# Performance work log

Hardware: AMD Instinct MI355X
Metric: run time of the kernel (lower is better)

The kernel has to match this reference:

```python
import jax, jax.numpy as jnp
import numpy as np

# Mamba2 config (from AdapterMamba: d_model=1024, n_layer=4, headdim=32; mamba_ssm defaults)
D_MODEL = 1024
N_LAYER = 4
EXPAND = 2
HEADDIM = 32
D_STATE = 128
D_CONV = 4
NGROUPS = 1
D_INNER = EXPAND * D_MODEL            # 2048
NHEADS = D_INNER // HEADDIM           # 64
CONV_DIM = D_INNER + 2 * NGROUPS * D_STATE   # 2304
D_IN_PROJ = 2 * D_INNER + 2 * NGROUPS * D_STATE + NHEADS  # 4416
BATCH, SEQLEN = 4, 2048


def setup_inputs() -> dict:
    key = jax.random.key(0)
    ks = jax.random.split(key, 8)
    x = jax.random.normal(ks[0], (BATCH, SEQLEN, D_MODEL), jnp.float32)
    s_in = 1.0 / np.sqrt(D_MODEL)
    s_out = 1.0 / np.sqrt(D_INNER)
    W_in = jax.random.normal(ks[1], (N_LAYER, D_MODEL, D_IN_PROJ), jnp.float32) * s_in
    conv_w = jax.random.normal(ks[2], (N_LAYER, CONV_DIM, D_CONV), jnp.float32) * 0.5
    conv_b = jnp.zeros((N_LAYER, CONV_DIM), jnp.float32)
    # dt_bias = softplus^{-1}(dt) for dt in [1e-3, 0.1] (mamba dt_init)
    dt = jax.random.uniform(ks[3], (N_LAYER, NHEADS), jnp.float32, 0.001, 0.1)
    dt_bias = jnp.log(jnp.expm1(dt))
    # A in [1, 16] per head (A_init_range)
    A_log = jnp.log(jax.random.uniform(ks[4], (N_LAYER, NHEADS), jnp.float32, 1.0, 16.0))
    D = jnp.ones((N_LAYER, NHEADS), jnp.float32)
    gate_norm_w = jnp.ones((N_LAYER, D_INNER), jnp.float32)
    W_out = jax.random.normal(ks[5], (N_LAYER, D_INNER, D_MODEL), jnp.float32) * s_out
    block_norm_w = jnp.ones((N_LAYER, D_MODEL), jnp.float32)
    final_norm_w = jnp.ones((D_MODEL,), jnp.float32)
    return dict(x=x, W_in=W_in, conv_w=conv_w, conv_b=conv_b, dt_bias=dt_bias,
                A_log=A_log, D=D, gate_norm_w=gate_norm_w, W_out=W_out,
                block_norm_w=block_norm_w, final_norm_w=final_norm_w)


def _rmsnorm(x, w, eps=1e-5):
    return x * jax.lax.rsqrt(jnp.mean(x * x, axis=-1, keepdims=True) + eps) * w


def _mamba2_layer(h, Wi, cw, cb, dtb, Alog, Dh, gw, Wo):
    B, L, _ = h.shape
    zxbcdt = h @ Wi                                        # [B,L,4416]
    z, xBC, dt = jnp.split(zxbcdt, [D_INNER, D_INNER + CONV_DIM], axis=-1)
    # causal depthwise conv1d, width D_CONV, over (x, B, C) channels
    xp = jnp.pad(xBC, ((0, 0), (D_CONV - 1, 0), (0, 0)))
    conv = cb + sum(xp[:, k:k + L, :] * cw[:, k] for k in range(D_CONV))
    xBC = jax.nn.silu(conv)
    xs, Bm, Cm = jnp.split(xBC, [D_INNER, D_INNER + D_STATE], axis=-1)
    xs = xs.reshape(B, L, NHEADS, HEADDIM)                 # [B,L,H,P]
    dt = jax.nn.softplus(dt + dtb)                         # [B,L,H]
    A = -jnp.exp(Alog)                                     # [H]
    dA = jnp.exp(dt * A)                                   # [B,L,H]
    dtx = dt[..., None] * xs                               # [B,L,H,P]

    def step(hs, inp):
        dA_t, dtx_t, B_t, C_t = inp
        # hs: [B,H,P,N]
        hs = hs * dA_t[:, :, None, None] + dtx_t[..., None] * B_t[:, None, None, :]
        y = jnp.einsum('bhpn,bn->bhp', hs, C_t)
        return hs, y

    h0 = jnp.zeros((B, NHEADS, HEADDIM, D_STATE), h.dtype)
    _, ys = jax.lax.scan(step, h0, (dA.swapaxes(0, 1), dtx.swapaxes(0, 1),
                                    Bm.swapaxes(0, 1), Cm.swapaxes(0, 1)))
    y = ys.swapaxes(0, 1) + Dh[None, None, :, None] * xs   # skip term D*x
    y = y.reshape(B, L, D_INNER)
    y = _rmsnorm(y * jax.nn.silu(z), gw)                   # gated RMSNorm (Mamba2)
    return y @ Wo


def reference(x, W_in, conv_w, conv_b, dt_bias, A_log, D, gate_norm_w, W_out,
              block_norm_w, final_norm_w):
    h = x
    for l in range(N_LAYER):
        h = h + _mamba2_layer(_rmsnorm(h, block_norm_w[l]), W_in[l], conv_w[l],
                              conv_b[l], dt_bias[l], A_log[l], D[l],
                              gate_norm_w[l], W_out[l])
    return _rmsnorm(h, final_norm_w)
```

## Files before the change

kernel.cpp:

```cpp
#include <hip/hip_runtime.h>

typedef unsigned short u16;
typedef __bf16 bf16x8 __attribute__((ext_vector_type(8)));
typedef float f32x4 __attribute__((ext_vector_type(4)));
typedef u16 u16x8 __attribute__((ext_vector_type(8)));

#define NLAYER 4
#define DMODEL 1024
#define DINNER 2048
#define NHEADS 64
#define CONVDIM 2304
#define XBCLD 2368
#define DPROJ 4416
#define DPROJP 4608
#define BATCH 4
#define SEQLEN 2048
#define NTOK 8192
#define QC 64
#define NCH (SEQLEN / QC)

__device__ __forceinline__ u16 f2bf(float f) {
  union { float f; unsigned u; } v; v.f = f;
  return (u16)((v.u + 0x7fffu + ((v.u >> 16) & 1u)) >> 16);
}
__device__ __forceinline__ float bf2f(u16 h) {
  union { unsigned u; float f; } v; v.u = (unsigned)h << 16; return v.f;
}

__device__ __forceinline__ float block_sum256(float v) {
  __shared__ float red[4];
  #pragma unroll
  for (int o = 32; o; o >>= 1) v += __shfl_xor(v, o);
  int t = threadIdx.x;
  if ((t & 63) == 0) red[t >> 6] = v;
  __syncthreads();
  return red[0] + red[1] + red[2] + red[3];
}

__device__ __forceinline__ int swz128(int row, int g) { return (row << 7) + (((g ^ (row & 7)) << 3)); }
__device__ __forceinline__ int swz64(int row, int g)  { return (row << 6) + (((g ^ (row & 7)) << 3)); }

#define GLDS16(g, s) __builtin_amdgcn_global_load_lds( \
    (const __attribute__((address_space(1))) void*)(g), \
    (__attribute__((address_space(3))) void*)(s), 16, 0, 0)

#define PH_READ(buf, p)                                                        \
  if ((p) == 0) {                                                              \
    _Pragma("unroll") for (int nf = 0; nf < NF; ++nf)                          \
    _Pragma("unroll") for (int ks = 0; ks < 2; ++ks)                           \
      breg[nf][ks] = readB(buf, nf, ks);                                       \
  }                                                                            \
  _Pragma("unroll") for (int i = 0; i < 2; ++i)                                \
  _Pragma("unroll") for (int ks = 0; ks < 2; ++ks)                             \
    ar[i][ks] = readA(buf, ((p) << 1) + i, ks);

#define PH_TAIL(buf, p)                                                        \
  __builtin_amdgcn_sched_barrier(0);                                           \
  __builtin_amdgcn_s_barrier();                                                \
  asm volatile("s_waitcnt lgkmcnt(0)" ::: "memory");                           \
  __builtin_amdgcn_sched_barrier(0);                                           \
  __builtin_amdgcn_s_setprio(1);                                               \
  _Pragma("unroll") for (int i = 0; i < 2; ++i)                                \
  _Pragma("unroll") for (int nf = 0; nf < NF; ++nf)                            \
  _Pragma("unroll") for (int ks = 0; ks < 2; ++ks)                             \
    acc[((p) << 1) + i][nf] = __builtin_amdgcn_mfma_f32_16x16x32_bf16(         \
        ar[i][ks], breg[nf][ks], acc[((p) << 1) + i][nf], 0, 0, 0);            \
  __builtin_amdgcn_s_setprio(0);                                               \
  __builtin_amdgcn_s_barrier();

template<int NF, int MODE>
__global__ __launch_bounds__(512, 1) void gemm8p_k(
    const u16* __restrict__ A, const u16* __restrict__ Bt,
    float* __restrict__ C, u16* __restrict__ zy, u16* __restrict__ xbc,
    float* __restrict__ dtraw, int K, int nt2) {
  constexpr int NBH = NF / 2;
  __shared__ __align__(16) u16 smem[(2 * (2 + NBH)) * 8192];

  const int tid = threadIdx.x;
  const int w = tid >> 6, l = tid & 63;
  const int wm = w >> 2, wn = w & 3;
  const int l16 = l & 15, kg = l >> 4;
  const int lr = l >> 3, lc = l & 7;
  const int swg = lc ^ lr;

  const int gx = gridDim.x;
  const int nwg = gx * gridDim.y;
  int bid = blockIdx.y * gx + blockIdx.x;
  bid = (bid & 7) * (nwg >> 3) + (bid >> 3);
  const int m0 = (bid / gx) << 8;
  const int n0 = (bid % gx) * (NF << 6);

  f32x4 acc[8][NF] = {};
  bf16x8 breg[NF][2];
  bf16x8 ar[2][2];

  auto stageA = [&](int buf, int h, int kt) {
    const size_t kb = (size_t)(kt << 6) + (swg << 3);
    u16* dst = smem + (((buf << 1) + h) << 13);
    #pragma unroll
    for (int j = 0; j < 2; ++j)
      GLDS16(A + (size_t)(m0 + (h << 7) + (j << 6) + (w << 3) + lr) * K + kb,
             dst + (j << 12) + (w << 9));
  };
  auto stageB = [&](int buf, int h, int kt) {
    const size_t kb = (size_t)(kt << 6) + (swg << 3);
    u16* dst = smem + ((4 + buf * NBH + h) << 13);
    #pragma unroll
    for (int j = 0; j < 2; ++j)
      GLDS16(Bt + (size_t)(n0 + (h << 7) + (j << 6) + (w << 3) + lr) * K + kb,
             dst + (j << 12) + (w << 9));
  };
  auto readA = [&](int buf, int mf, int ks) -> bf16x8 {
    const int r = (mf << 4) + l16;
    return *(const bf16x8*)&smem[(((buf << 1) + wm) << 13) + (r << 6) + ((((ks << 2) + kg) ^ (r & 7)) << 3)];
  };
  auto readB = [&](int buf, int nf, int ks) -> bf16x8 {
    const int row = wn * (NF << 4) + (nf << 4) + l16;
    const int bh = row >> 7, r = row & 127;
    return *(const bf16x8*)&smem[((4 + buf * NBH + bh) << 13) + (r << 6) + ((((ks << 2) + kg) ^ (r & 7)) << 3)];
  };

  stageA(0, 0, 0); stageA(0, 1, 0);
  #pragma unroll
  for (int h = 0; h < NBH; ++h) stageB(0, h, 0);
  #pragma unroll
  for (int h = 0; h < NBH; ++h) stageB(1, h, 1);
  asm volatile("s_waitcnt vmcnt(0)" ::: "memory");
  __syncthreads();

  for (int t = 0; t < nt2; ++t) {
    const int kt0 = t << 1;
    const bool more = (t + 1 < nt2);
    PH_READ(0, 0)
    stageA(1, 0, kt0 + 1);
    PH_TAIL(0, 0)
    PH_READ(0, 1)
    stageA(1, 1, kt0 + 1);
    PH_TAIL(0, 1)
    PH_READ(0, 2)
    if (more) stageB(0, 0, kt0 + 2);
    PH_TAIL(0, 2)
    PH_READ(0, 3)
    if (more && NBH == 2) stageB(0, 1, kt0 + 2);
    if (more) { asm volatile("s_waitcnt vmcnt(%0)" :: "n"(2 * NBH) : "memory"); }
    else      { asm volatile("s_waitcnt vmcnt(0)" ::: "memory"); }
    PH_TAIL(0, 3)
    PH_READ(1, 0)
    if (more) stageA(0, 0, kt0 + 2);
    PH_TAIL(1, 0)
    PH_READ(1, 1)
    if (more) stageA(0, 1, kt0 + 2);
    PH_TAIL(1, 1)
    PH_READ(1, 2)
    if (more) stageB(1, 0, kt0 + 3);
    PH_TAIL(1, 2)
    PH_READ(1, 3)
    if (more && NBH == 2) stageB(1, 1, kt0 + 3);
    if (more) { asm volatile("s_waitcnt vmcnt(%0)" :: "n"(2 * NBH) : "memory"); }
    PH_TAIL(1, 3)
  }

  __syncthreads();
  if (MODE == 1) {
    const int nt = n0 >> 8;
    if (nt == 17) {
      if (wn == 0) {
        #pragma unroll
        for (int mf = 0; mf < 8; ++mf) {
          const int row = m0 + (wm << 7) + (mf << 4) + (kg << 2);
          #pragma unroll
          for (int nf = 0; nf < NF; ++nf) {
            const int dc = (nf << 4) + l16;
            #pragma unroll
            for (int r = 0; r < 4; ++r)
              dtraw[(size_t)(row + r) * 64 + dc] = acc[mf][nf][r];
          }
        }
      }
    } else {
      #pragma unroll
      for (int mf = 0; mf < 8; ++mf) {
        #pragma unroll
        for (int nf = 0; nf < NF; ++nf) {
          const int col = (wn << 6) + (nf << 4) + l16;
          #pragma unroll
          for (int r = 0; r < 4; ++r) {
            const int row = (wm << 7) + (mf << 4) + (kg << 2) + r;
            smem[(row << 8) + (((col >> 3) ^ (row & 7)) << 3) + (col & 7)] = f2bf(acc[mf][nf][r]);
          }
        }
      }
      __syncthreads();
      const int g = l & 31;
      #pragma unroll
      for (int j = 0; j < 16; ++j) {
        const int row = (w << 5) + (j << 1) + (l >> 5);
        u16x8 v = *(const u16x8*)&smem[(row << 8) + ((g ^ (row & 7)) << 3)];
        const size_t grow = (size_t)(m0 + row);
        const int gcol = n0 + (g << 3);
        if (nt < 8) *(u16x8*)&zy[grow * DINNER + gcol] = v;
        else        *(u16x8*)&xbc[grow * XBCLD + (gcol - 2048)] = v;
      }
    }
  } else {
    float* smf = (float*)smem;
    #pragma unroll
    for (int pass = 0; pass < 2; ++pass) {
      if (wm == pass) {
        #pragma unroll
        for (int mf = 0; mf < 8; ++mf) {
          #pragma unroll
          for (int nf = 0; nf < NF; ++nf) {
            const int col = (wn << 5) + (nf << 4) + l16;
            #pragma unroll
            for (int r = 0; r < 4; ++r) {
              const int lrow = (mf << 4) + (kg << 2) + r;
              smf[(lrow << 7) + (((col >> 2) ^ (lrow & 7)) << 2) + (col & 3)] = acc[mf][nf][r];
            }
          }
        }
      }
      __syncthreads();
      const int g = l & 31;
      #pragma unroll
      for (int j = 0; j < 8; ++j) {
        const int lrow = (w << 4) + (j << 1) + (l >> 5);
        f32x4 v = *(const f32x4*)&smf[(lrow << 7) + ((g ^ (lrow & 7)) << 2)];
        float* cp = &C[(size_t)(m0 + (pass << 7) + lrow) * DMODEL + n0 + (g << 2)];
        f32x4 o = *(const f32x4*)cp;
        #pragma unroll
        for (int q = 0; q < 4; ++q) o[q] += v[q];
        *(f32x4*)cp = o;
      }
      __syncthreads();
    }
  }
}

__global__ __launch_bounds__(256) void transpose_cvt_k(
    const float* __restrict__ in, u16* __restrict__ out, int R, int Cin, int Cpad) {
  __shared__ float t[64][65];
  const int c0 = blockIdx.x << 6, r0 = blockIdx.y << 6;
  const int tx = threadIdx.x & 63, ty = threadIdx.x >> 6;
  #pragma unroll
  for (int i = 0; i < 16; ++i) {
    int r = ty + (i << 2);
    int cc = c0 + tx;
    t[r][tx] = (cc < Cin) ? in[(size_t)(r0 + r) * Cin + cc] : 0.f;
  }
  __syncthreads();
  #pragma unroll
  for (int i = 0; i < 16; ++i) {
    int c = ty + (i << 2);
    out[(size_t)(c0 + c) * R + r0 + tx] = f2bf(t[tx][c]);
  }
}

__global__ __launch_bounds__(256) void transpose_bf16_k(
    const u16* __restrict__ in, u16* __restrict__ out) {
  __shared__ __align__(16) u16 tl[64][72];
  const int c0 = blockIdx.x << 6, r0 = blockIdx.y << 6;
  const int tid = threadIdx.x;
  #pragma unroll
  for (int i = 0; i < 2; ++i) {
    int row = (tid >> 3) + (i << 5);
    int cs = tid & 7;
    *(int4*)&tl[row][cs << 3] =
        *(const int4*)&in[(size_t)(r0 + row) * CONVDIM + c0 + (cs << 3)];
  }
  __syncthreads();
  #pragma unroll
  for (int p = 0; p < 2; ++p) {
    int slot = tid + (p << 8);
    int c = slot >> 3, tb = slot & 7;
    u16x8 v;
    #pragma unroll
    for (int j = 0; j < 8; ++j) v[j] = tl[(tb << 3) + j][c];
    *(u16x8*)&out[(size_t)(c0 + c) * NTOK + r0 + (tb << 3)] = v;
  }
}

__global__ void copy_k(const float* __restrict__ in, float* __restrict__ out, int n4) {
  int i = blockIdx.x * blockDim.x + threadIdx.x;
  int stride = gridDim.x * blockDim.x;
  for (; i < n4; i += stride)
    *(f32x4*)&out[(size_t)i * 4] = *(const f32x4*)&in[(size_t)i * 4];
}

__global__ __launch_bounds__(256) void rmsnorm_bf16_k(
    const float* __restrict__ in, const float* __restrict__ w, u16* __restrict__ out) {
  const size_t row = blockIdx.x;
  const int t = threadIdx.x;
  f32x4 v = *(const f32x4*)&in[row * DMODEL + t * 4];
  float ss = block_sum256(v[0]*v[0] + v[1]*v[1] + v[2]*v[2] + v[3]*v[3]);
  float sc = rsqrtf(ss * (1.f / DMODEL) + 1e-5f);
  f32x4 wv = *(const f32x4*)&w[t * 4];
  ushort4 o;
  o.x = f2bf(v[0] * sc * wv[0]); o.y = f2bf(v[1] * sc * wv[1]);
  o.z = f2bf(v[2] * sc * wv[2]); o.w = f2bf(v[3] * sc * wv[3]);
  *(ushort4*)&out[row * DMODEL + t * 4] = o;
}

__global__ __launch_bounds__(256) void final_rmsnorm_k(
    const float* __restrict__ in, const float* __restrict__ w, float* __restrict__ out) {
  const size_t row = blockIdx.x;
  const int t = threadIdx.x;
  f32x4 v = *(const f32x4*)&in[row * DMODEL + t * 4];
  float ss = block_sum256(v[0]*v[0] + v[1]*v[1] + v[2]*v[2] + v[3]*v[3]);
  float sc = rsqrtf(ss * (1.f / DMODEL) + 1e-5f);
  f32x4 wv = *(const f32x4*)&w[t * 4];
  f32x4 o;
  #pragma unroll
  for (int j = 0; j < 4; ++j) o[j] = v[j] * sc * wv[j];
  *(f32x4*)&out[row * DMODEL + t * 4] = o;
}

__global__ __launch_bounds__(256) void conv_silu_k(
    const u16* __restrict__ xbc, const float* __restrict__ cw,
    const float* __restrict__ cb, u16* __restrict__ xact) {
  const int c = (blockIdx.x << 8) + threadIdx.x;
  const int b = blockIdx.y >> 8;
  const int t0 = (blockIdx.y & 255) << 3;
  const size_t rb = (size_t)b * SEQLEN + t0;
  const float w0 = cw[c*4], w1 = cw[c*4+1], w2 = cw[c*4+2], w3 = cw[c*4+3];
  const float bias = cb[c];
  const u16* src = xbc + c;
  float xm3 = t0 ? bf2f(src[(rb - 3) * XBCLD]) : 0.f;
  float xm2 = t0 ? bf2f(src[(rb - 2) * XBCLD]) : 0.f;
  float xm1 = t0 ? bf2f(src[(rb - 1) * XBCLD]) : 0.f;
  #pragma unroll
  for (int j = 0; j < 8; ++j) {
    float xc = bf2f(src[(rb + j) * XBCLD]);
    float a = bias + w0 * xm3 + w1 * xm2 + w2 * xm1 + w3 * xc;
    xact[(rb + j) * CONVDIM + c] = f2bf(a / (1.f + expf(-a)));
    xm3 = xm2; xm2 = xm1; xm1 = xc;
  }
}

__global__ __launch_bounds__(256, 2) void ssd_local_k(
    const u16* __restrict__ xact, const u16* __restrict__ XT,
    const u16* __restrict__ BT, const float* __restrict__ dtraw,
    const float* __restrict__ dt_bias, const float* __restrict__ A_log,
    const float* __restrict__ Dv, u16* __restrict__ ybuf,
    u16* __restrict__ Sg, float* __restrict__ etg, float* __restrict__ decayg) {
  __shared__ __align__(16) u16 Bs[64 * 128];
  __shared__ __align__(16) u16 U[128 * 64];
  __shared__ __align__(16) u16 Xt[32 * 64];
  __shared__ __align__(16) u16 Pl[64 * 64];
  __shared__ float cums[64], dts[64], fac[64];

  const int h = blockIdx.x, ch = blockIdx.y, b = blockIdx.z;
  const int tid = threadIdx.x, w = tid >> 6, l = tid & 63;
  const int l16 = l & 15, kg = l >> 4;
  const size_t tokb = (size_t)b * SEQLEN + (ch << 6);
  const size_t schunk = ((size_t)(b * 64 + h) << 5) + ch;

  const int srow = tid >> 2, sseg = tid & 3;
  int4 creg[4], breg[4], btreg[4];
  #pragma unroll
  for (int i = 0; i < 4; ++i) {
    creg[i] = *(const int4*)&xact[(tokb + srow) * CONVDIM + 2176 + (sseg << 5) + (i << 3)];
    breg[i] = *(const int4*)&xact[(tokb + srow) * CONVDIM + 2048 + (sseg << 5) + (i << 3)];
  }
  const int xrow = tid >> 3, xseg = tid & 7;
  int4 xreg = *(const int4*)&XT[(size_t)((h << 5) + xrow) * NTOK + tokb + (xseg << 3)];
  #pragma unroll
  for (int i = 0; i < 4; ++i)
    btreg[i] = *(const int4*)&BT[(size_t)(tid >> 1) * NTOK + tokb + ((((tid & 1) << 2) + i) << 3)];

  #pragma unroll
  for (int i = 0; i < 4; ++i) {
    *(int4*)&U[swz128(srow, (sseg << 2) + i)]  = creg[i];
    *(int4*)&Bs[swz128(srow, (sseg << 2) + i)] = breg[i];
  }
  *(int4*)&Xt[swz64(xrow, xseg)] = xreg;

  if (w == 0) {
    float raw = dtraw[(tokb + l) * 64 + h] + dt_bias[h];
    float dtv = raw > 20.f ? raw : log1pf(__expf(raw));
    float cv = -dtv * __expf(A_log[h]);
    #pragma unroll
    for (int d = 1; d < 64; d <<= 1) {
      float o = __shfl_up(cv, d);
      if (l >= d) cv += o;
    }
    float a63 = __shfl(cv, 63);
    cums[l] = cv; dts[l] = dtv; fac[l] = dtv * __expf(a63 - cv);
    etg[(schunk << 6) + l] = __expf(cv);
    if (l == 0) decayg[schunk] = __expf(a63);
  }
  const float Dh = Dv[h];
  __syncthreads();

  f32x4 gacc[4] = {};
  #pragma unroll
  for (int ks = 0; ks < 4; ++ks) {
    bf16x8 ac = *(const bf16x8*)&U[swz128((w << 4) + l16, (ks << 2) + kg)];
    #pragma unroll
    for (int j = 0; j < 4; ++j)
      if (j <= w) {
        bf16x8 bb = *(const bf16x8*)&Bs[swz128((j << 4) + l16, (ks << 2) + kg)];
        gacc[j] = __builtin_amdgcn_mfma_f32_16x16x32_bf16(ac, bb, gacc[j], 0, 0, 0);
      }
  }
  float c_t[4];
  #pragma unroll
  for (int r = 0; r < 4; ++r) c_t[r] = cums[(w << 4) + (kg << 2) + r];
  #pragma unroll
  for (int j = 0; j < 4; ++j) {
    const int s = (j << 4) + l16;
    const float c_s = cums[s], d_s = dts[s];
    #pragma unroll
    for (int r = 0; r < 4; ++r) {
      const int t = (w << 4) + (kg << 2) + r;
      float v = (s <= t) ? gacc[j][r] * __expf(c_t[r] - c_s) * d_s : 0.f;
      Pl[(t << 6) + ((((s >> 3) ^ (t & 7)) << 3) | (s & 7))] = f2bf(v);
    }
  }

  f32x4 y1[2] = {};
  const int nks = (w >> 1) + 1;
  for (int ks = 0; ks < nks; ++ks) {
    bf16x8 ap = *(const bf16x8*)&Pl[swz64((w << 4) + l16, (ks << 2) + kg)];
    #pragma unroll
    for (int pj = 0; pj < 2; ++pj) {
      bf16x8 bx = *(const bf16x8*)&Xt[swz64((pj << 4) + l16, (ks << 2) + kg)];
      y1[pj] = __builtin_amdgcn_mfma_f32_16x16x32_bf16(ap, bx, y1[pj], 0, 0, 0);
    }
  }
  #pragma unroll
  for (int r = 0; r < 4; ++r) {
    const int t = (w << 4) + (kg << 2) + r;
    #pragma unroll
    for (int pj = 0; pj < 2; ++pj) {
      const int p = (pj << 4) + l16;
      float xv = bf2f(Xt[(p << 6) + ((((t >> 3) ^ (p & 7)) << 3) | (t & 7))]);
      ybuf[(tokb + t) * DINNER + (h << 5) + p] = f2bf(y1[pj][r] + Dh * xv);
    }
  }

  __syncthreads();
  #pragma unroll
  for (int i = 0; i < 4; ++i)
    *(int4*)&U[swz64(tid >> 1, ((tid & 1) << 2) + i)] = btreg[i];
  __syncthreads();

  f32x4 sacc[2][2] = {};
  #pragma unroll
  for (int ks = 0; ks < 2; ++ks) {
    float f8[8];
    #pragma unroll
    for (int j = 0; j < 8; ++j) f8[j] = fac[(ks << 5) + (kg << 3) + j];
    #pragma unroll
    for (int pt = 0; pt < 2; ++pt) {
      bf16x8 xr = *(const bf16x8*)&Xt[swz64((pt << 4) + l16, (ks << 2) + kg)];
      bf16x8 xs;
      #pragma unroll
      for (int j = 0; j < 8; ++j) xs[j] = (__bf16)((float)xr[j] * f8[j]);
      #pragma unroll
      for (int nt = 0; nt < 2; ++nt) {
        bf16x8 bb = *(const bf16x8*)&U[swz64(((w << 1) + nt) * 16 + l16, (ks << 2) + kg)];
        sacc[pt][nt] = __builtin_amdgcn_mfma_f32_16x16x32_bf16(xs, bb, sacc[pt][nt], 0, 0, 0);
      }
    }
  }
  u16* sp = Sg + (schunk << 12);
  #pragma unroll
  for (int pt = 0; pt < 2; ++pt)
    #pragma unroll
    for (int nt = 0; nt < 2; ++nt)
      #pragma unroll
      for (int r = 0; r < 4; ++r) {
        const int pr = (pt << 4) + (kg << 2) + r;
        const int n = (w << 5) + (nt << 4) + l16;
        sp[(pr << 7) + n] = f2bf(sacc[pt][nt][r]);
      }
}

__global__ __launch_bounds__(256) void state_scan_k(
    u16* __restrict__ SH, const float* __restrict__ decayg) {
  const int bid = blockIdx.x;
  const size_t base = ((size_t)bid << 17) + ((size_t)threadIdx.x << 4);
  float acc[16] = {};
  u16x8 s0 = *(const u16x8*)&SH[base];
  u16x8 s1 = *(const u16x8*)&SH[base + 8];
  for (int ch = 0; ch < 32; ++ch) {
    const float d = decayg[(bid << 5) + ch];
    u16x8 n0 = {}, n1 = {};
    if (ch + 1 < 32) {
      n0 = *(const u16x8*)&SH[base + ((size_t)(ch + 1) << 12)];
      n1 = *(const u16x8*)&SH[base + ((size_t)(ch + 1) << 12) + 8];
    }
    u16x8 h0, h1;
    #pragma unroll
    for (int j = 0; j < 8; ++j) { h0[j] = f2bf(acc[j]); h1[j] = f2bf(acc[8 + j]); }
    *(u16x8*)&SH[base + ((size_t)ch << 12)] = h0;
    *(u16x8*)&SH[base + ((size_t)ch << 12) + 8] = h1;
    #pragma unroll
    for (int j = 0; j < 8; ++j) {
      acc[j]     = d * acc[j]     + bf2f(s0[j]);
      acc[8 + j] = d * acc[8 + j] + bf2f(s1[j]);
    }
    s0 = n0; s1 = n1;
  }
}

__global__ __launch_bounds__(256) void ssd_cross_k(
    const u16* __restrict__ xact, const u16* __restrict__ Hg,
    const float* __restrict__ etg, u16* __restrict__ ybuf) {
  __shared__ __align__(16) u16 Cs[64 * 128];
  __shared__ __align__(16) u16 Hb[32 * 128];
  __shared__ float etl[64];
  const int h = blockIdx.x, ch = blockIdx.y + 1, b = blockIdx.z;
  const int tid = threadIdx.x, w = tid >> 6, l = tid & 63;
  const int l16 = l & 15, kg = l >> 4;
  const size_t tokb = (size_t)b * SEQLEN + (ch << 6);
  const size_t schunk = ((size_t)(b * 64 + h) << 5) + ch;

  const int srow = tid >> 2, sseg = tid & 3;
  #pragma unroll
  for (int i = 0; i < 4; ++i) {
    int4 v = *(const int4*)&xact[(tokb + srow) * CONVDIM + 2176 + (sseg << 5) + (i << 3)];
    *(int4*)&Cs[swz128(srow, (sseg << 2) + i)] = v;
  }
  const int hp = tid >> 3, hseg = tid & 7;
  #pragma unroll
  for (int i = 0; i < 2; ++i) {
    int4 v = *(const int4*)&Hg[(schunk << 12) + (hp << 7) + (((hseg << 1) + i) << 3)];
    *(int4*)&Hb[swz128(hp, (hseg << 1) + i)] = v;
  }
  if (tid < 64) etl[tid] = etg[(schunk << 6) + tid];
  __syncthreads();

  f32x4 y2[2] = {};
  #pragma unroll
  for (int ks = 0; ks < 4; ++ks) {
    bf16x8 ac = *(const bf16x8*)&Cs[swz128((w << 4) + l16, (ks << 2) + kg)];
    #pragma unroll
    for (int pj = 0; pj < 2; ++pj) {
      bf16x8 bh = *(const bf16x8*)&Hb[swz128((pj << 4) + l16, (ks << 2) + kg)];
      y2[pj] = __builtin_amdgcn_mfma_f32_16x16x32_bf16(ac, bh, y2[pj], 0, 0, 0);
    }
  }
  #pragma unroll
  for (int r = 0; r < 4; ++r) {
    const int t = (w << 4) + (kg << 2) + r;
    const float et = etl[t];
    #pragma unroll
    for (int pj = 0; pj < 2; ++pj) {
      const int p = (pj << 4) + l16;
      const size_t a = (tokb + t) * DINNER + (h << 5) + p;
      ybuf[a] = f2bf(bf2f(ybuf[a]) + et * y2[pj][r]);
    }
  }
}

__global__ __launch_bounds__(256) void gate_rmsnorm_k(
    const u16* __restrict__ y, u16* __restrict__ zy, const float* __restrict__ gw) {
  const size_t row = blockIdx.x;
  const int t = threadIdx.x;
  bf16x8 yv = *(const bf16x8*)&y[row * DINNER + t * 8];
  bf16x8 zv = *(const bf16x8*)&zy[row * DINNER + t * 8];
  float val[8]; float ss = 0.f;
  #pragma unroll
  for (int j = 0; j < 8; ++j) {
    float z = (float)zv[j];
    float v = (float)yv[j] * (z / (1.f + expf(-z)));
    val[j] = v; ss += v * v;
  }
  ss = block_sum256(ss);
  float sc = rsqrtf(ss * (1.f / DINNER) + 1e-5f);
  ushort4 o0, o1;
  o0.x = f2bf(val[0]*sc*gw[t*8+0]); o0.y = f2bf(val[1]*sc*gw[t*8+1]);
  o0.z = f2bf(val[2]*sc*gw[t*8+2]); o0.w = f2bf(val[3]*sc*gw[t*8+3]);
  o1.x = f2bf(val[4]*sc*gw[t*8+4]); o1.y = f2bf(val[5]*sc*gw[t*8+5]);
  o1.z = f2bf(val[6]*sc*gw[t*8+6]); o1.w = f2bf(val[7]*sc*gw[t*8+7]);
  *(ushort4*)&zy[row * DINNER + t * 8] = o0;
  *(ushort4*)&zy[row * DINNER + t * 8 + 4] = o1;
}

extern "C" void kernel_launch(void* const* d_in, const int* in_sizes, int n_in,
                              void* d_out, int out_size, void* d_ws, size_t ws_size,
                              hipStream_t stream) {
  const float* x       = (const float*)d_in[0];
  const float* W_in    = (const float*)d_in[1];
  const float* conv_w  = (const float*)d_in[2];
  const float* conv_b  = (const float*)d_in[3];
  const float* dt_bias = (const float*)d_in[4];
  const float* A_log   = (const float*)d_in[5];
  const float* Dv      = (const float*)d_in[6];
  const float* gate_w  = (const float*)d_in[7];
  const float* W_out   = (const float*)d_in[8];
  const float* block_w = (const float*)d_in[9];
  const float* final_w = (const float*)d_in[10];
  float* out = (float*)d_out;

  char* p = (char*)d_ws;
  auto alloc = [&](size_t bytes) { char* r = p; p += (bytes + 255) & ~(size_t)255; return r; };
  float* hbuf  = (float*)alloc((size_t)NTOK * DMODEL * 4);
  u16*   slabA = (u16*)  alloc((size_t)NTOK * DINNER * 2);
  u16*   slabB = (u16*)  alloc((size_t)NTOK * DINNER * 2);
  u16*   slabC = (u16*)  alloc((size_t)NTOK * CONVDIM * 2);
  u16*   xbcXT = (u16*)  alloc((size_t)NTOK * XBCLD * 2);
  float* dtraw = (float*)alloc((size_t)NTOK * NHEADS * 4);
  u16*   BT    = (u16*)  alloc((size_t)128 * NTOK * 2);
  if ((size_t)(p - (char*)d_ws) > ws_size) return;

  u16*   Sg     = (u16*)  alloc((size_t)BATCH * NHEADS * NCH * 4096 * 2);
  float* etg    = (float*)alloc((size_t)BATCH * NHEADS * NCH * 64 * 4);
  float* decayg = (float*)alloc((size_t)BATCH * NHEADS * NCH * 4);
  const bool par = ((size_t)(p - (char*)d_ws) <= ws_size);

  u16* hn   = slabA;
  u16* ybuf = slabA;
  u16* wt   = slabC;
  u16* xact = slabC;
  u16* xbc  = xbcXT;
  u16* XT   = xbcXT;

  copy_k<<<2048, 256, 0, stream>>>(x, hbuf, NTOK * DMODEL / 4);

  for (int l = 0; l < NLAYER; ++l) {
    rmsnorm_bf16_k<<<NTOK, 256, 0, stream>>>(hbuf, block_w + l * DMODEL, hn);
    transpose_cvt_k<<<dim3(DPROJP/64, DMODEL/64), 256, 0, stream>>>(
        W_in + (size_t)l * DMODEL * DPROJ, wt, DMODEL, DPROJ, DPROJP);
    gemm8p_k<4, 1><<<dim3(DPROJP/256, NTOK/256), 512, 0, stream>>>(
        hn, wt, nullptr, slabB, xbc, dtraw, DMODEL, DMODEL / 128);
    conv_silu_k<<<dim3(CONVDIM/256, BATCH * SEQLEN / 8), 256, 0, stream>>>(
        xbc, conv_w + (size_t)l * CONVDIM * 4, conv_b + (size_t)l * CONVDIM, xact);
    transpose_bf16_k<<<dim3(DINNER/64, NTOK/64), 256, 0, stream>>>(xact, XT);
    transpose_bf16_k<<<dim3(2, NTOK/64), 256, 0, stream>>>(xact + DINNER, BT);
    if (par) {
      ssd_local_k<<<dim3(NHEADS, NCH, BATCH), 256, 0, stream>>>(
          xact, XT, BT, dtraw, dt_bias + l * NHEADS, A_log + l * NHEADS,
          Dv + l * NHEADS, ybuf, Sg, etg, decayg);
      state_scan_k<<<BATCH * NHEADS, 256, 0, stream>>>(Sg, decayg);
      ssd_cross_k<<<dim3(NHEADS, NCH - 1, BATCH), 256, 0, stream>>>(
          xact, Sg, etg, ybuf);
    }
    gate_rmsnorm_k<<<NTOK, 256, 0, stream>>>(ybuf, slabB, gate_w + (size_t)l * DINNER);
    transpose_cvt_k<<<dim3(DMODEL/64, DINNER/64), 256, 0, stream>>>(
        W_out + (size_t)l * DINNER * DMODEL, wt, DINNER, DMODEL, DMODEL);
    gemm8p_k<2, 0><<<dim3(DMODEL/128, NTOK/256), 512, 0, stream>>>(
        slabB, wt, hbuf, nullptr, nullptr, nullptr, DINNER, DINNER / 128);
  }
  final_rmsnorm_k<<<NTOK, 256, 0, stream>>>(hbuf, final_w, out);
}
```

Baseline: 1.512 ms.

## Fuse conv+SiLU with B transpose, drop X transpose, relax GEMM prologue wait

Replaces the conv_silu kernel and two transpose kernels with a single tiled conv_tr kernel. It stages a 64x64 token-channel tile in LDS, computes the causal conv+SiLU, writes xact, and for the B channels also writes the transposed BT. ssd_local now reads X directly from xact and transposes it into LDS with scalar stores, so the separate XT transpose pass and its global round trip go away. The GEMM prologue now waits only for the first stage's loads before the barrier instead of all loads. The costs are scattered 2-byte LDS writes in ssd_local and a more complex conv kernel.

```diff
diff --git a/kernel.cpp b/kernel.cpp
--- a/kernel.cpp
+++ b/kernel.cpp
@@ -125,8 +125,9 @@
   for (int h = 0; h < NBH; ++h) stageB(0, h, 0);
   #pragma unroll
   for (int h = 0; h < NBH; ++h) stageB(1, h, 1);
-  asm volatile("s_waitcnt vmcnt(0)" ::: "memory");
-  __syncthreads();
+  asm volatile("s_waitcnt vmcnt(%0) lgkmcnt(0)" :: "n"(2 * NBH) : "memory");
+  __builtin_amdgcn_sched_barrier(0);
+  __builtin_amdgcn_s_barrier();
 
   for (int t = 0; t < nt2; ++t) {
     const int kt0 = t << 1;
@@ -256,30 +257,6 @@
   }
 }
 
-__global__ __launch_bounds__(256) void transpose_bf16_k(
-    const u16* __restrict__ in, u16* __restrict__ out) {
-  __shared__ __align__(16) u16 tl[64][72];
-  const int c0 = blockIdx.x << 6, r0 = blockIdx.y << 6;
-  const int tid = threadIdx.x;
-  #pragma unroll
-  for (int i = 0; i < 2; ++i) {
-    int row = (tid >> 3) + (i << 5);
-    int cs = tid & 7;
-    *(int4*)&tl[row][cs << 3] =
-        *(const int4*)&in[(size_t)(r0 + row) * CONVDIM + c0 + (cs << 3)];
-  }
-  __syncthreads();
-  #pragma unroll
-  for (int p = 0; p < 2; ++p) {
-    int slot = tid + (p << 8);
-    int c = slot >> 3, tb = slot & 7;
-    u16x8 v;
-    #pragma unroll
-    for (int j = 0; j < 8; ++j) v[j] = tl[(tb << 3) + j][c];
-    *(u16x8*)&out[(size_t)(c0 + c) * NTOK + r0 + (tb << 3)] = v;
-  }
-}
-
 __global__ void copy_k(const float* __restrict__ in, float* __restrict__ out, int n4) {
   int i = blockIdx.x * blockDim.x + threadIdx.x;
   int stride = gridDim.x * blockDim.x;
@@ -315,34 +292,82 @@
   *(f32x4*)&out[row * DMODEL + t * 4] = o;
 }
 
-__global__ __launch_bounds__(256) void conv_silu_k(
+__global__ __launch_bounds__(256) void conv_tr_k(
     const u16* __restrict__ xbc, const float* __restrict__ cw,
-    const float* __restrict__ cb, u16* __restrict__ xact) {
-  const int c = (blockIdx.x << 8) + threadIdx.x;
-  const int b = blockIdx.y >> 8;
-  const int t0 = (blockIdx.y & 255) << 3;
-  const size_t rb = (size_t)b * SEQLEN + t0;
-  const float w0 = cw[c*4], w1 = cw[c*4+1], w2 = cw[c*4+2], w3 = cw[c*4+3];
-  const float bias = cb[c];
-  const u16* src = xbc + c;
-  float xm3 = t0 ? bf2f(src[(rb - 3) * XBCLD]) : 0.f;
-  float xm2 = t0 ? bf2f(src[(rb - 2) * XBCLD]) : 0.f;
-  float xm1 = t0 ? bf2f(src[(rb - 1) * XBCLD]) : 0.f;
+    const float* __restrict__ cb, u16* __restrict__ xact, u16* __restrict__ BT) {
+  __shared__ __align__(16) u16 xin[67][72];
+  __shared__ __align__(16) u16 xtr[64][72];
+  const int ch0 = blockIdx.x << 6, tok0 = blockIdx.y << 6;
+  const int tid = threadIdx.x;
+  const bool bstart = (tok0 & (SEQLEN - 1)) == 0;
+  {
+    const int rr = tid >> 3, sg = (tid & 7) << 3;
+    #pragma unroll
+    for (int i = 0; i < 2; ++i) {
+      int r = rr + (i << 5);
+      if (bstart && r < 3) *(u16x8*)&xin[r][sg] = (u16x8){};
+      else *(int4*)&xin[r][sg] = *(const int4*)&xbc[(size_t)(tok0 - 3 + r) * XBCLD + ch0 + sg];
+    }
+    if (tid < 24) {
+      int r = 64 + (tid >> 3), s2 = (tid & 7) << 3;
+      *(int4*)&xin[r][s2] = *(const int4*)&xbc[(size_t)(tok0 - 3 + r) * XBCLD + ch0 + s2];
+    }
+  }
+  __syncthreads();
+  const int c2 = tid & 31, th = tid >> 5;
+  const int c = c2 << 1, tb = th << 3;
+  float wv[2][4], bias[2];
+  #pragma unroll
+  for (int cc = 0; cc < 2; ++cc) {
+    bias[cc] = cb[ch0 + c + cc];
+    #pragma unroll
+    for (int k = 0; k < 4; ++k) wv[cc][k] = cw[(ch0 + c + cc) * 4 + k];
+  }
+  float m3[2], m2[2], m1[2];
+  #pragma unroll
+  for (int cc = 0; cc < 2; ++cc) {
+    m3[cc] = bf2f(xin[tb][c + cc]);
+    m2[cc] = bf2f(xin[tb + 1][c + cc]);
+    m1[cc] = bf2f(xin[tb + 2][c + cc]);
+  }
+  u16 ov[8][2];
   #pragma unroll
   for (int j = 0; j < 8; ++j) {
-    float xc = bf2f(src[(rb + j) * XBCLD]);
-    float a = bias + w0 * xm3 + w1 * xm2 + w2 * xm1 + w3 * xc;
-    xact[(rb + j) * CONVDIM + c] = f2bf(a / (1.f + expf(-a)));
-    xm3 = xm2; xm2 = xm1; xm1 = xc;
+    #pragma unroll
+    for (int cc = 0; cc < 2; ++cc) {
+      float xc = bf2f(xin[tb + 3 + j][c + cc]);
+      float a = bias[cc] + wv[cc][0]*m3[cc] + wv[cc][1]*m2[cc] + wv[cc][2]*m1[cc] + wv[cc][3]*xc;
+      ov[j][cc] = f2bf(a / (1.f + expf(-a)));
+      m3[cc] = m2[cc]; m2[cc] = m1[cc]; m1[cc] = xc;
+    }
+    unsigned pk = (unsigned)ov[j][0] | ((unsigned)ov[j][1] << 16);
+    *(unsigned*)&xact[(size_t)(tok0 + tb + j) * CONVDIM + ch0 + c] = pk;
+  }
+  if (ch0 == 2048 || ch0 == 2112) {
+    #pragma unroll
+    for (int cc = 0; cc < 2; ++cc) {
+      u16x8 v;
+      #pragma unroll
+      for (int j = 0; j < 8; ++j) v[j] = ov[j][cc];
+      *(u16x8*)&xtr[c + cc][tb] = v;
+    }
+    __syncthreads();
+    #pragma unroll
+    for (int p = 0; p < 2; ++p) {
+      int slot = tid + (p << 8);
+      int cc2 = slot >> 3, tseg = slot & 7;
+      u16x8 v = *(const u16x8*)&xtr[cc2][tseg << 3];
+      *(u16x8*)&BT[(size_t)(ch0 - 2048 + cc2) * NTOK + tok0 + (tseg << 3)] = v;
+    }
   }
 }
 
 __global__ __launch_bounds__(256, 2) void ssd_local_k(
-    const u16* __restrict__ xact, const u16* __restrict__ XT,
-    const u16* __restrict__ BT, const float* __restrict__ dtraw,
-    const float* __restrict__ dt_bias, const float* __restrict__ A_log,
-    const float* __restrict__ Dv, u16* __restrict__ ybuf,
-    u16* __restrict__ Sg, float* __restrict__ etg, float* __restrict__ decayg) {
+    const u16* __restrict__ xact, const u16* __restrict__ BT,
+    const float* __restrict__ dtraw, const float* __restrict__ dt_bias,
+    const float* __restrict__ A_log, const float* __restrict__ Dv,
+    u16* __restrict__ ybuf, u16* __restrict__ Sg,
+    float* __restrict__ etg, float* __restrict__ decayg) {
   __shared__ __align__(16) u16 Bs[64 * 128];
   __shared__ __align__(16) u16 U[128 * 64];
   __shared__ __align__(16) u16 Xt[32 * 64];
@@ -362,8 +387,8 @@
     creg[i] = *(const int4*)&xact[(tokb + srow) * CONVDIM + 2176 + (sseg << 5) + (i << 3)];
     breg[i] = *(const int4*)&xact[(tokb + srow) * CONVDIM + 2048 + (sseg << 5) + (i << 3)];
   }
-  const int xrow = tid >> 3, xseg = tid & 7;
-  int4 xreg = *(const int4*)&XT[(size_t)((h << 5) + xrow) * NTOK + tokb + (xseg << 3)];
+  const int xtt = tid >> 2, xps = tid & 3;
+  int4 xreg = *(const int4*)&xact[(tokb + xtt) * CONVDIM + (h << 5) + (xps << 3)];
   #pragma unroll
   for (int i = 0; i < 4; ++i)
     btreg[i] = *(const int4*)&BT[(size_t)(tid >> 1) * NTOK + tokb + ((((tid & 1) << 2) + i) << 3)];
@@ -373,7 +398,14 @@
     *(int4*)&U[swz128(srow, (sseg << 2) + i)]  = creg[i];
     *(int4*)&Bs[swz128(srow, (sseg << 2) + i)] = breg[i];
   }
-  *(int4*)&Xt[swz64(xrow, xseg)] = xreg;
+  {
+    u16x8 xv = *(const u16x8*)&xreg;
+    #pragma unroll
+    for (int j = 0; j < 8; ++j) {
+      const int pp = (xps << 3) + j;
+      Xt[(pp << 6) + ((((xtt >> 3) ^ (pp & 7)) << 3) | (xtt & 7))] = xv[j];
+    }
+  }
 
   if (w == 0) {
     float raw = dtraw[(tokb + l) * 64 + h] + dt_bias[h];
@@ -601,7 +633,7 @@
   u16*   slabA = (u16*)  alloc((size_t)NTOK * DINNER * 2);
   u16*   slabB = (u16*)  alloc((size_t)NTOK * DINNER * 2);
   u16*   slabC = (u16*)  alloc((size_t)NTOK * CONVDIM * 2);
-  u16*   xbcXT = (u16*)  alloc((size_t)NTOK * XBCLD * 2);
+  u16*   xbc   = (u16*)  alloc((size_t)NTOK * XBCLD * 2);
   float* dtraw = (float*)alloc((size_t)NTOK * NHEADS * 4);
   u16*   BT    = (u16*)  alloc((size_t)128 * NTOK * 2);
   if ((size_t)(p - (char*)d_ws) > ws_size) return;
@@ -615,8 +647,6 @@
   u16* ybuf = slabA;
   u16* wt   = slabC;
   u16* xact = slabC;
-  u16* xbc  = xbcXT;
-  u16* XT   = xbcXT;
 
   copy_k<<<2048, 256, 0, stream>>>(x, hbuf, NTOK * DMODEL / 4);
 
@@ -626,13 +656,11 @@
         W_in + (size_t)l * DMODEL * DPROJ, wt, DMODEL, DPROJ, DPROJP);
     gemm8p_k<4, 1><<<dim3(DPROJP/256, NTOK/256), 512, 0, stream>>>(
         hn, wt, nullptr, slabB, xbc, dtraw, DMODEL, DMODEL / 128);
-    conv_silu_k<<<dim3(CONVDIM/256, BATCH * SEQLEN / 8), 256, 0, stream>>>(
-        xbc, conv_w + (size_t)l * CONVDIM * 4, conv_b + (size_t)l * CONVDIM, xact);
-    transpose_bf16_k<<<dim3(DINNER/64, NTOK/64), 256, 0, stream>>>(xact, XT);
-    transpose_bf16_k<<<dim3(2, NTOK/64), 256, 0, stream>>>(xact + DINNER, BT);
+    conv_tr_k<<<dim3(CONVDIM/64, NTOK/64), 256, 0, stream>>>(
+        xbc, conv_w + (size_t)l * CONVDIM * 4, conv_b + (size_t)l * CONVDIM, xact, BT);
     if (par) {
       ssd_local_k<<<dim3(NHEADS, NCH, BATCH), 256, 0, stream>>>(
-          xact, XT, BT, dtraw, dt_bias + l * NHEADS, A_log + l * NHEADS,
+          xact, BT, dtraw, dt_bias + l * NHEADS, A_log + l * NHEADS,
           Dv + l * NHEADS, ybuf, Sg, etg, decayg);
       state_scan_k<<<BATCH * NHEADS, 256, 0, stream>>>(Sg, decayg);
       ssd_cross_k<<<dim3(NHEADS, NCH - 1, BATCH), 256, 0, stream>>>(
```

Result: faster. 1.479 ms (-2.2%).
